# Kernel tuning notes

Measured on AMD Instinct MI355X. Metric: run time of the kernel, lower is better.

The kernel has to match this reference:

```python
import jax, jax.numpy as jnp
import numpy as np

NUM_HEADS = 8
DIM = 256
SCALE = (DIM // NUM_HEADS) ** -0.5  # head_dim = dim // nhead = 32


def setup_inputs() -> dict:
    key = jax.random.key(0)
    k1, k2, k3, k4, k5 = jax.random.split(key, 5)
    B, N = 1, 4096
    qk = jax.random.normal(k1, (B, N, 3 * DIM), dtype=jnp.float32)
    v_cls = jax.random.normal(k2, (B, N, 2 * DIM), dtype=jnp.float32)
    masks = jax.random.uniform(k3, (B, N, N), dtype=jnp.float32)
    # torch Linear weights stored as [in, out] for x @ W
    W_qk = jax.random.normal(k4, (3 * DIM, 6 * DIM), dtype=jnp.float32) * (3 * DIM) ** -0.5
    W_v = jax.random.normal(k5, (2 * DIM, 2 * DIM), dtype=jnp.float32) * (2 * DIM) ** -0.5
    return {"qk": qk, "v_cls": v_cls, "masks": masks, "W_qk": W_qk, "W_v": W_v}


def reference(qk, v_cls, masks, W_qk, W_v):
    B, N, C_qk = qk.shape
    C_cls = v_cls.shape[-1]
    H = NUM_HEADS
    hd_qk = C_qk // H   # 96
    hd_v = C_cls // H   # 64

    # qk projection: [B,N,6*dim] -> (2,B,H,N,hd_qk)
    proj = (qk @ W_qk).reshape(B, N, 2, H, hd_qk).transpose(2, 0, 3, 1, 4)
    q, k = proj[0], proj[1]                      # [B,H,N,hd_qk]
    v = (v_cls @ W_v).reshape(B, N, H, hd_v).transpose(0, 2, 1, 3)  # [B,H,N,hd_v]

    attn = jnp.einsum('bhnd,bhmd->bhnm', q, k) * SCALE
    attn = jax.nn.softmax(attn, axis=-1)

    # post-softmax mask-mul and renorm by mask-sum and head count
    m = masks[:, None]                           # [B,1,N,N] broadcast over heads
    attn = attn * m / (H * jnp.sum(m, axis=-1, keepdims=True))
    # attn_drop with p=0.0 is identity in eval

    x_cls = jnp.einsum('bhnm,bhmd->bhnd', attn, v)
    return x_cls.transpose(0, 2, 1, 3).reshape(B, N, C_cls)
```

## Files before the change

kernel.cpp:

```cpp
#include <hip/hip_runtime.h>

typedef __attribute__((ext_vector_type(8))) _Float16 half8;
typedef __attribute__((ext_vector_type(4))) _Float16 half4;
typedef __attribute__((ext_vector_type(2))) _Float16 half2;
typedef __attribute__((ext_vector_type(2))) __fp16 fp16x2;
typedef __attribute__((ext_vector_type(4))) float f32x4;

#define N_SEQ 4096
#define HD_QK 96
#define HD_V  64
#define NHEADS 8
#define QSCALE 0.25505545556f
#define ESHIFT 8.0f

union PKC { fp16x2 p; half2 h; };

__device__ inline half2 pk_cvt(float a, float b) {
    PKC u;
    u.p = __builtin_amdgcn_cvt_pkrtz(a, b);
    return u.h;
}

__device__ inline half8 cvt8(float4 a, float4 b) {
    half8 h;
    h[0] = (_Float16)a.x; h[1] = (_Float16)a.y; h[2] = (_Float16)a.z; h[3] = (_Float16)a.w;
    h[4] = (_Float16)b.x; h[5] = (_Float16)b.y; h[6] = (_Float16)b.z; h[7] = (_Float16)b.w;
    return h;
}

__device__ inline void cast_blk(const float* __restrict__ in, _Float16* __restrict__ out,
                                int blk, int t) {
    size_t i = ((size_t)blk * 256 + t) * 8;
    float4 a = *(const float4*)(in + i);
    float4 b = *(const float4*)(in + i + 4);
    *(half8*)(out + i) = cvt8(a, b);
}

__global__ __launch_bounds__(256) void prep(
    const float* __restrict__ qk, const float* __restrict__ v_cls,
    const float* __restrict__ masks, const float* __restrict__ W_qk,
    const float* __restrict__ W_v,
    _Float16* __restrict__ Xh, _Float16* __restrict__ Vch,
    _Float16* __restrict__ Msw, float* __restrict__ Msum,
    _Float16* __restrict__ Wqkt, _Float16* __restrict__ Wvt)
{
    __shared__ float tile[32][33];
    const int bx = blockIdx.x, t = threadIdx.x;
    if (bx < 1536) {
        cast_blk(qk, Xh, bx, t);
    } else if (bx < 2560) {
        cast_blk(v_cls, Vch, bx - 1536, t);
    } else if (bx < 3968) {
        const bool big = bx < 3712;
        const int id = big ? bx - 2560 : bx - 3712;
        const int nx = big ? 48 : 16;
        const int C = big ? 1536 : 512, R = big ? 768 : 512;
        const float* in = big ? W_qk : W_v;
        _Float16* out = big ? Wqkt : Wvt;
        int cx = id % nx, cy = id / nx;
        int tx = t & 31, ty = t >> 5;
        int c0 = cx * 32, r0 = cy * 32;
        for (int k = 0; k < 4; k++)
            tile[ty + 8 * k][tx] = in[(size_t)(r0 + ty + 8 * k) * C + c0 + tx];
        __syncthreads();
        for (int k = 0; k < 4; k++)
            out[(size_t)(c0 + ty + 8 * k) * R + r0 + tx] = (_Float16)tile[tx][ty + 8 * k];
    } else {
        const int m = bx - 3968;
        const int q = m >> 1;
        const int k0 = (m & 1) * 2048 + t * 8;
        const float* src = masks + (size_t)q * N_SEQ + k0;
        float4 a = *(const float4*)src;
        float4 b = *(const float4*)(src + 4);
        const int q0b = q >> 6, l15 = q & 15, nt = (q >> 4) & 3;
        const int kb = k0 >> 6, wsl = (k0 >> 4) & 3, qd = (k0 >> 2) & 3;
        _Float16* dst = Msw + ((size_t)(q0b * 64 + kb) * 4 + wsl) * 1024
                            + l15 * 64 + qd * 16 + nt * 4;
        half4 h0 = {(_Float16)a.x, (_Float16)a.y, (_Float16)a.z, (_Float16)a.w};
        half4 h1 = {(_Float16)b.x, (_Float16)b.y, (_Float16)b.z, (_Float16)b.w};
        *(half4*)dst = h0;
        *(half4*)(dst + 16) = h1;
        float s = (a.x + a.y) + (a.z + a.w) + (b.x + b.y) + (b.z + b.w);
        for (int off = 1; off < 64; off <<= 1) s += __shfl_xor(s, off);
        if ((t & 63) == 0) atomicAdd(&Msum[q], s);
    }
}

__global__ __launch_bounds__(256) void proj_fused(
    const _Float16* __restrict__ Xh, const _Float16* __restrict__ Vch,
    const _Float16* __restrict__ Wqkt, const _Float16* __restrict__ Wvt,
    _Float16* __restrict__ Qh, _Float16* __restrict__ Kh,
    _Float16* __restrict__ Vtg)
{
    __shared__ _Float16 smem[2 * 128 * 72];
    _Float16 (*Xs)[72] = (_Float16 (*)[72])smem;
    _Float16 (*Ws)[72] = (_Float16 (*)[72])(smem + 128 * 72);

    const int t = threadIdx.x;
    const int lane = t & 63, wv = t >> 6;
    const int quad = lane >> 4, l15 = lane & 15;
    const bool qkmode = blockIdx.x < 12;
    const int n0 = qkmode ? blockIdx.x * 128 : (blockIdx.x - 12) * 128;
    const int row0 = blockIdx.y * 128;
    const int K = qkmode ? 768 : 512;
    const _Float16* X = qkmode ? Xh : Vch;
    const _Float16* Wt = qkmode ? Wqkt : Wvt;

    const int mB = (wv & 1) * 64, nB = (wv >> 1) * 64;
    const int sr = t >> 1, sk = (t & 1) * 32;

    const f32x4 fzero = {0.f, 0.f, 0.f, 0.f};
    f32x4 acc[4][4];
    for (int i = 0; i < 4; i++)
        for (int j = 0; j < 4; j++) acc[i][j] = fzero;

    for (int k0 = 0; k0 < K; k0 += 64) {
        __syncthreads();
        {
            const _Float16* xp = X + (size_t)(row0 + sr) * K + k0 + sk;
            *(half8*)&Xs[sr][sk]      = *(const half8*)xp;
            *(half8*)&Xs[sr][sk + 8]  = *(const half8*)(xp + 8);
            *(half8*)&Xs[sr][sk + 16] = *(const half8*)(xp + 16);
            *(half8*)&Xs[sr][sk + 24] = *(const half8*)(xp + 24);
            const _Float16* wp = Wt + (size_t)(n0 + sr) * K + k0 + sk;
            *(half8*)&Ws[sr][sk]      = *(const half8*)wp;
            *(half8*)&Ws[sr][sk + 8]  = *(const half8*)(wp + 8);
            *(half8*)&Ws[sr][sk + 16] = *(const half8*)(wp + 16);
            *(half8*)&Ws[sr][sk + 24] = *(const half8*)(wp + 24);
        }
        __syncthreads();
        for (int c = 0; c < 2; c++) {
            half8 af[4], bf[4];
            for (int i = 0; i < 4; i++)
                af[i] = *(const half8*)&Xs[mB + 16 * i + l15][c * 32 + quad * 8];
            for (int j = 0; j < 4; j++)
                bf[j] = *(const half8*)&Ws[nB + 16 * j + l15][c * 32 + quad * 8];
            for (int i = 0; i < 4; i++)
                for (int j = 0; j < 4; j++)
                    acc[i][j] = __builtin_amdgcn_mfma_f32_16x16x32_f16(af[i], bf[j], acc[i][j], 0, 0, 0);
        }
    }

    __syncthreads();
    _Float16 (*Ct)[136] = (_Float16 (*)[136])smem;
    for (int j = 0; j < 4; j++) {
        int col = n0 + nB + 16 * j + l15;
        float scl = (qkmode && col < 768) ? QSCALE : 1.0f;
        for (int i = 0; i < 4; i++)
            for (int r = 0; r < 4; r++)
                Ct[mB + 16 * i + quad * 4 + r][nB + 16 * j + l15] =
                    (_Float16)(acc[i][j][r] * scl);
    }
    __syncthreads();

    if (qkmode) {
        for (int e = 0; e < 8; e++) {
            int id = e * 256 + t;
            int row = id >> 4, cc = id & 15;
            int col = n0 + cc * 8;
            int w = col >= 768 ? 1 : 0;
            int rem = col - w * 768;
            int h = rem / 96, d = rem - h * 96;
            _Float16* dst = w ? Kh : Qh;
            *(half8*)&dst[((size_t)h * N_SEQ + row0 + row) * HD_QK + d] =
                *(const half8*)&Ct[row][cc * 8];
        }
    } else {
        for (int e = 0; e < 4; e++) {
            int id = e * 256 + t;
            int col = id >> 3, rc = id & 7;
            int c = n0 + col;
            int h = c >> 6, d = c & 63;
            half8 v0, v1;
            for (int k = 0; k < 8; k++) {
                v0[k] = Ct[rc * 16 + k][col];
                v1[k] = Ct[rc * 16 + 8 + k][col];
            }
            _Float16* dst = &Vtg[((size_t)h * HD_V + d) * N_SEQ + row0 + rc * 16];
            *(half8*)dst = v0;
            *(half8*)(dst + 8) = v1;
        }
    }
}

__global__ __launch_bounds__(256, 3) void flash_attn(
    const _Float16* __restrict__ Qh, const _Float16* __restrict__ Kh,
    const _Float16* __restrict__ Vtg, const _Float16* __restrict__ Msw,
    _Float16* __restrict__ Owsh, float* __restrict__ Lws)
{
    __shared__ __align__(16) float Ob[2][64][68];
    __shared__ float Lb[2][64];

    const int t = threadIdx.x;
    const int lane = t & 63, w = t >> 6;
    const int quad = lane >> 4, l15 = lane & 15;
    const int bx = blockIdx.x;
    const int q0b = bx & 63;
    const int hz = bx >> 6;
    const int head = hz & 7;
    const int z = hz >> 3;
    const int q0 = q0b * 64;
    const int kb0 = 21 * z, kbE = (z == 2) ? 64 : kb0 + 21;

    half8 qf[3][4];
    for (int nt = 0; nt < 4; nt++) {
        const _Float16* qp = Qh + ((size_t)head * N_SEQ + q0 + 16 * nt + l15) * HD_QK + 8 * quad;
        for (int c = 0; c < 3; c++)
            qf[c][nt] = *(const half8*)(qp + 32 * c);
    }

    const _Float16* kbase = Kh + ((size_t)head * N_SEQ + 16 * w + l15) * HD_QK + 8 * quad;
    const _Float16* vbase = Vtg + ((size_t)head * HD_V + l15) * N_SEQ + 16 * w + 4 * quad;
    const _Float16* mbase = Msw + ((size_t)(q0b * 64 + kb0) * 4 + w) * 1024
                                + (l15 * 4 + quad) * 16;

    const f32x4 fzero = {0.f, 0.f, 0.f, 0.f};
    f32x4 oacc[4][4];
    for (int nt = 0; nt < 4; nt++)
        for (int v = 0; v < 4; v++) oacc[nt][v] = fzero;
    float lsum[4] = {0.f, 0.f, 0.f, 0.f};

    half8 kf[3];
    half4 vf[4];
    half8 m01, m23;
    {
        const _Float16* kp = kbase + (size_t)kb0 * 64 * HD_QK;
        for (int c = 0; c < 3; c++) kf[c] = *(const half8*)(kp + 32 * c);
        const _Float16* vp = vbase + kb0 * 64;
        for (int v = 0; v < 4; v++) vf[v] = *(const half4*)(vp + (size_t)(16 * v) * N_SEQ);
        m01 = *(const half8*)mbase;
        m23 = *(const half8*)(mbase + 8);
    }

    for (int kb = kb0; kb < kbE; kb++) {
        const int kn = (kb + 1 < kbE) ? kb + 1 : kb;

        f32x4 sT[4];
        for (int nt = 0; nt < 4; nt++) sT[nt] = fzero;
        for (int c = 0; c < 3; c++)
            for (int nt = 0; nt < 4; nt++)
                sT[nt] = __builtin_amdgcn_mfma_f32_16x16x32_f16(kf[c], qf[c][nt], sT[nt], 0, 0, 0);
        {
            const _Float16* kp = kbase + (size_t)kn * 64 * HD_QK;
            for (int c = 0; c < 3; c++) kf[c] = *(const half8*)(kp + 32 * c);
        }

        half4 af[4];
        {
            half2 mh[8];
            for (int i = 0; i < 4; i++) {
                mh[i]     = half2{m01[2 * i], m01[2 * i + 1]};
                mh[4 + i] = half2{m23[2 * i], m23[2 * i + 1]};
            }
            for (int nt = 0; nt < 4; nt++) {
                float p0 = exp2f(sT[nt][0] - ESHIFT);
                float p1 = exp2f(sT[nt][1] - ESHIFT);
                float p2 = exp2f(sT[nt][2] - ESHIFT);
                float p3 = exp2f(sT[nt][3] - ESHIFT);
                lsum[nt] += (p0 + p1) + (p2 + p3);
                half2 lo = pk_cvt(p0, p1) * mh[2 * nt];
                half2 hi = pk_cvt(p2, p3) * mh[2 * nt + 1];
                af[nt] = half4{lo[0], lo[1], hi[0], hi[1]};
            }
        }
        {
            const _Float16* mp = mbase + (size_t)(kn - kb0) * 4096;
            m01 = *(const half8*)mp;
            m23 = *(const half8*)(mp + 8);
        }

        for (int nt = 0; nt < 4; nt++)
            for (int v = 0; v < 4; v++)
                oacc[nt][v] = __builtin_amdgcn_mfma_f32_16x16x16f16(af[nt], vf[v], oacc[nt][v], 0, 0, 0);
        {
            const _Float16* vp = vbase + kn * 64;
            for (int v = 0; v < 4; v++) vf[v] = *(const half4*)(vp + (size_t)(16 * v) * N_SEQ);
        }
    }

    for (int nt = 0; nt < 4; nt++) {
        lsum[nt] += __shfl_xor(lsum[nt], 16);
        lsum[nt] += __shfl_xor(lsum[nt], 32);
    }

    if (w & 1) {
        for (int nt = 0; nt < 4; nt++) {
            for (int v = 0; v < 4; v++)
                for (int r = 0; r < 4; r++)
                    Ob[w >> 1][16 * nt + 4 * quad + r][16 * v + l15] = oacc[nt][v][r];
            if (quad == 0) Lb[w >> 1][16 * nt + l15] = lsum[nt];
        }
    }
    __syncthreads();
    if (!(w & 1)) {
        for (int nt = 0; nt < 4; nt++) {
            for (int v = 0; v < 4; v++)
                for (int r = 0; r < 4; r++)
                    Ob[w >> 1][16 * nt + 4 * quad + r][16 * v + l15] += oacc[nt][v][r];
            if (quad == 0) Lb[w >> 1][16 * nt + l15] += lsum[nt];
        }
    }
    __syncthreads();

    {
        int row = t >> 2, c0 = (t & 3) * 16;
        _Float16* obase = Owsh + (size_t)z * N_SEQ * 512 + (size_t)(q0 + row) * 512
                          + head * HD_V + c0;
        for (int g = 0; g < 2; g++) {
            half8 h;
            for (int j = 0; j < 8; j++)
                h[j] = (_Float16)(Ob[0][row][c0 + 8 * g + j] + Ob[1][row][c0 + 8 * g + j]);
            *(half8*)(obase + 8 * g) = h;
        }
        if (t < 64)
            Lws[((size_t)z * NHEADS + head) * N_SEQ + q0 + t] = Lb[0][t] + Lb[1][t];
    }
}

__global__ __launch_bounds__(256) void finalize(
    const _Float16* __restrict__ Owsh, const float* __restrict__ Lws,
    const float* __restrict__ Msum, float* __restrict__ out)
{
    const size_t ZSTR = (size_t)N_SEQ * 512;
    size_t o = ((size_t)blockIdx.x * 256 + threadIdx.x) * 8;
    int q = (int)(o >> 9);
    int head = (int)((o & 511) >> 6);
    half8 p0 = *(const half8*)(Owsh + o);
    half8 p1 = *(const half8*)(Owsh + ZSTR + o);
    half8 p2 = *(const half8*)(Owsh + 2 * ZSTR + o);
    float l = Lws[(size_t)head * N_SEQ + q]
            + Lws[((size_t)NHEADS + head) * N_SEQ + q]
            + Lws[((size_t)2 * NHEADS + head) * N_SEQ + q];
    float inv = 1.0f / (l * (float)NHEADS * Msum[q]);
    float4 r0, r1;
    r0.x = ((float)p0[0] + (float)p1[0] + (float)p2[0]) * inv;
    r0.y = ((float)p0[1] + (float)p1[1] + (float)p2[1]) * inv;
    r0.z = ((float)p0[2] + (float)p1[2] + (float)p2[2]) * inv;
    r0.w = ((float)p0[3] + (float)p1[3] + (float)p2[3]) * inv;
    r1.x = ((float)p0[4] + (float)p1[4] + (float)p2[4]) * inv;
    r1.y = ((float)p0[5] + (float)p1[5] + (float)p2[5]) * inv;
    r1.z = ((float)p0[6] + (float)p1[6] + (float)p2[6]) * inv;
    r1.w = ((float)p0[7] + (float)p1[7] + (float)p2[7]) * inv;
    *(float4*)(out + o) = r0;
    *(float4*)(out + o + 4) = r1;
}

extern "C" void kernel_launch(void* const* d_in, const int* in_sizes, int n_in,
                              void* d_out, int out_size, void* d_ws, size_t ws_size,
                              hipStream_t stream) {
    const float* qk    = (const float*)d_in[0];
    const float* v_cls = (const float*)d_in[1];
    const float* masks = (const float*)d_in[2];
    const float* W_qk  = (const float*)d_in[3];
    const float* W_v   = (const float*)d_in[4];
    float* out = (float*)d_out;

    char* wsp = (char*)d_ws;
    _Float16* Xh   = (_Float16*)(wsp);
    _Float16* Vch  = (_Float16*)(wsp + (size_t)6291456);
    _Float16* Wqkt = (_Float16*)(wsp + (size_t)10485760);
    _Float16* Wvt  = (_Float16*)(wsp + (size_t)12845056);
    _Float16* Owsh = (_Float16*)(wsp);
    size_t off = 13631488;
    auto allocB = [&](size_t bytes) { char* p = wsp + off; off += (bytes + 255) & ~(size_t)255; return p; };
    _Float16* Qh   = (_Float16*)allocB((size_t)NHEADS * N_SEQ * HD_QK * 2);
    _Float16* Kh   = (_Float16*)allocB((size_t)NHEADS * N_SEQ * HD_QK * 2);
    _Float16* Vtg  = (_Float16*)allocB((size_t)NHEADS * HD_V * N_SEQ * 2);
    _Float16* Msw  = (_Float16*)allocB((size_t)N_SEQ * N_SEQ * 2);
    float*    Msum = (float*)allocB((size_t)N_SEQ * 4);
    float*    Lws  = (float*)allocB((size_t)3 * NHEADS * N_SEQ * 4);
    (void)ws_size;

    dim3 blk(256);
    (void)hipMemsetAsync(Msum, 0, N_SEQ * sizeof(float), stream);
    prep<<<dim3(12160), blk, 0, stream>>>(
        qk, v_cls, masks, W_qk, W_v, Xh, Vch, Msw, Msum, Wqkt, Wvt);

    proj_fused<<<dim3(16, N_SEQ / 128), blk, 0, stream>>>(
        Xh, Vch, Wqkt, Wvt, Qh, Kh, Vtg);

    flash_attn<<<dim3(1536), blk, 0, stream>>>(
        Qh, Kh, Vtg, Msw, Owsh, Lws);

    finalize<<<dim3((N_SEQ * 512) / (256 * 8)), blk, 0, stream>>>(
        Owsh, Lws, Msum, out);
}
```

Measured before the change: 280.1 us.

## Rework mask prep tiling, shrink projection tiles with prefetch, split attention four ways

The mask conversion now processes whole 64x64 tiles through shared memory, so global writes are coalesced and one atomic is issued per row quarter instead of per wavefront. The projection kernel uses 64-row tiles with register prefetch of the next K slice and a higher occupancy hint. Flash attention splits the key range into four equal chunks instead of three uneven ones and raises occupancy to 4 blocks per CU. Finalize reduces over four partials. The workspace offset grows to hold the larger partial buffer. Risks are more partial traffic in finalize and register pressure under the tighter launch bounds.

```diff
diff --git a/kernel.cpp b/kernel.cpp
--- a/kernel.cpp
+++ b/kernel.cpp
@@ -12,8 +12,10 @@
 #define NHEADS 8
 #define QSCALE 0.25505545556f
 #define ESHIFT 8.0f
+#define NZ 4
 
 union PKC { fp16x2 p; half2 h; };
+union H8H2 { half8 v; half2 h2[4]; };
 
 __device__ inline half2 pk_cvt(float a, float b) {
     PKC u;
@@ -45,6 +47,7 @@
     _Float16* __restrict__ Wqkt, _Float16* __restrict__ Wvt)
 {
     __shared__ float tile[32][33];
+    __shared__ _Float16 Ml[64][68];
     const int bx = blockIdx.x, t = threadIdx.x;
     if (bx < 1536) {
         cast_blk(qk, Xh, bx, t);
@@ -66,76 +69,104 @@
         for (int k = 0; k < 4; k++)
             out[(size_t)(c0 + ty + 8 * k) * R + r0 + tx] = (_Float16)tile[tx][ty + 8 * k];
     } else {
-        const int m = bx - 3968;
-        const int q = m >> 1;
-        const int k0 = (m & 1) * 2048 + t * 8;
-        const float* src = masks + (size_t)q * N_SEQ + k0;
-        float4 a = *(const float4*)src;
-        float4 b = *(const float4*)(src + 4);
-        const int q0b = q >> 6, l15 = q & 15, nt = (q >> 4) & 3;
-        const int kb = k0 >> 6, wsl = (k0 >> 4) & 3, qd = (k0 >> 2) & 3;
-        _Float16* dst = Msw + ((size_t)(q0b * 64 + kb) * 4 + wsl) * 1024
-                            + l15 * 64 + qd * 16 + nt * 4;
-        half4 h0 = {(_Float16)a.x, (_Float16)a.y, (_Float16)a.z, (_Float16)a.w};
-        half4 h1 = {(_Float16)b.x, (_Float16)b.y, (_Float16)b.z, (_Float16)b.w};
-        *(half4*)dst = h0;
-        *(half4*)(dst + 16) = h1;
-        float s = (a.x + a.y) + (a.z + a.w) + (b.x + b.y) + (b.z + b.w);
-        for (int off = 1; off < 64; off <<= 1) s += __shfl_xor(s, off);
-        if ((t & 63) == 0) atomicAdd(&Msum[q], s);
-    }
-}
-
-__global__ __launch_bounds__(256) void proj_fused(
+        const int b = bx - 3968;
+        const int q0b6 = b >> 6, kb = b & 63;
+        const int qr = t >> 2, ks = t & 3;
+        const float* src = masks + (size_t)(q0b6 * 64 + qr) * N_SEQ + kb * 64 + ks * 16;
+        float4 a0 = *(const float4*)src;
+        float4 a1 = *(const float4*)(src + 4);
+        float4 a2 = *(const float4*)(src + 8);
+        float4 a3 = *(const float4*)(src + 12);
+        *(half8*)&Ml[qr][ks * 16]     = cvt8(a0, a1);
+        *(half8*)&Ml[qr][ks * 16 + 8] = cvt8(a2, a3);
+        float s = ((a0.x + a0.y) + (a0.z + a0.w)) + ((a1.x + a1.y) + (a1.z + a1.w))
+                + ((a2.x + a2.y) + (a2.z + a2.w)) + ((a3.x + a3.y) + (a3.z + a3.w));
+        s += __shfl_xor(s, 1);
+        s += __shfl_xor(s, 2);
+        if ((t & 3) == 0) atomicAdd(&Msum[q0b6 * 64 + qr], s);
+        __syncthreads();
+        const int wsl = t >> 6, l15 = (t >> 2) & 15, quad = t & 3;
+        _Float16* dst = Msw + ((size_t)(q0b6 * 64 + kb) * 4 + wsl) * 1024
+                            + l15 * 64 + quad * 16;
+        half8 o0, o1;
+        for (int nt = 0; nt < 2; nt++)
+            for (int j = 0; j < 4; j++)
+                o0[nt * 4 + j] = Ml[nt * 16 + l15][wsl * 16 + quad * 4 + j];
+        for (int nt = 2; nt < 4; nt++)
+            for (int j = 0; j < 4; j++)
+                o1[(nt - 2) * 4 + j] = Ml[nt * 16 + l15][wsl * 16 + quad * 4 + j];
+        *(half8*)dst = o0;
+        *(half8*)(dst + 8) = o1;
+    }
+}
+
+__global__ __launch_bounds__(256, 4) void proj_fused(
     const _Float16* __restrict__ Xh, const _Float16* __restrict__ Vch,
     const _Float16* __restrict__ Wqkt, const _Float16* __restrict__ Wvt,
     _Float16* __restrict__ Qh, _Float16* __restrict__ Kh,
     _Float16* __restrict__ Vtg)
 {
-    __shared__ _Float16 smem[2 * 128 * 72];
+    __shared__ _Float16 smem[64 * 72 + 128 * 72];
     _Float16 (*Xs)[72] = (_Float16 (*)[72])smem;
-    _Float16 (*Ws)[72] = (_Float16 (*)[72])(smem + 128 * 72);
+    _Float16 (*Ws)[72] = (_Float16 (*)[72])(smem + 64 * 72);
 
     const int t = threadIdx.x;
     const int lane = t & 63, wv = t >> 6;
     const int quad = lane >> 4, l15 = lane & 15;
     const bool qkmode = blockIdx.x < 12;
     const int n0 = qkmode ? blockIdx.x * 128 : (blockIdx.x - 12) * 128;
-    const int row0 = blockIdx.y * 128;
+    const int row0 = blockIdx.y * 64;
     const int K = qkmode ? 768 : 512;
     const _Float16* X = qkmode ? Xh : Vch;
     const _Float16* Wt = qkmode ? Wqkt : Wvt;
 
-    const int mB = (wv & 1) * 64, nB = (wv >> 1) * 64;
-    const int sr = t >> 1, sk = (t & 1) * 32;
+    const int mB = (wv & 1) * 32, nB = (wv >> 1) * 64;
+    const int xr = t >> 2, xc = (t & 3) * 16;
+    const int wr = t >> 1, wc = (t & 1) * 32;
 
     const f32x4 fzero = {0.f, 0.f, 0.f, 0.f};
-    f32x4 acc[4][4];
-    for (int i = 0; i < 4; i++)
+    f32x4 acc[2][4];
+    for (int i = 0; i < 2; i++)
         for (int j = 0; j < 4; j++) acc[i][j] = fzero;
+
+    half8 xg0, xg1, wg0, wg1, wg2, wg3;
+    {
+        const _Float16* xp = X + (size_t)(row0 + xr) * K + xc;
+        xg0 = *(const half8*)xp;
+        xg1 = *(const half8*)(xp + 8);
+        const _Float16* wp = Wt + (size_t)(n0 + wr) * K + wc;
+        wg0 = *(const half8*)wp;
+        wg1 = *(const half8*)(wp + 8);
+        wg2 = *(const half8*)(wp + 16);
+        wg3 = *(const half8*)(wp + 24);
+    }
 
     for (int k0 = 0; k0 < K; k0 += 64) {
         __syncthreads();
-        {
-            const _Float16* xp = X + (size_t)(row0 + sr) * K + k0 + sk;
-            *(half8*)&Xs[sr][sk]      = *(const half8*)xp;
-            *(half8*)&Xs[sr][sk + 8]  = *(const half8*)(xp + 8);
-            *(half8*)&Xs[sr][sk + 16] = *(const half8*)(xp + 16);
-            *(half8*)&Xs[sr][sk + 24] = *(const half8*)(xp + 24);
-            const _Float16* wp = Wt + (size_t)(n0 + sr) * K + k0 + sk;
-            *(half8*)&Ws[sr][sk]      = *(const half8*)wp;
-            *(half8*)&Ws[sr][sk + 8]  = *(const half8*)(wp + 8);
-            *(half8*)&Ws[sr][sk + 16] = *(const half8*)(wp + 16);
-            *(half8*)&Ws[sr][sk + 24] = *(const half8*)(wp + 24);
-        }
+        *(half8*)&Xs[xr][xc]     = xg0;
+        *(half8*)&Xs[xr][xc + 8] = xg1;
+        *(half8*)&Ws[wr][wc]      = wg0;
+        *(half8*)&Ws[wr][wc + 8]  = wg1;
+        *(half8*)&Ws[wr][wc + 16] = wg2;
+        *(half8*)&Ws[wr][wc + 24] = wg3;
         __syncthreads();
+        if (k0 + 64 < K) {
+            const _Float16* xp = X + (size_t)(row0 + xr) * K + k0 + 64 + xc;
+            xg0 = *(const half8*)xp;
+            xg1 = *(const half8*)(xp + 8);
+            const _Float16* wp = Wt + (size_t)(n0 + wr) * K + k0 + 64 + wc;
+            wg0 = *(const half8*)wp;
+            wg1 = *(const half8*)(wp + 8);
+            wg2 = *(const half8*)(wp + 16);
+            wg3 = *(const half8*)(wp + 24);
+        }
         for (int c = 0; c < 2; c++) {
-            half8 af[4], bf[4];
-            for (int i = 0; i < 4; i++)
+            half8 af[2], bf[4];
+            for (int i = 0; i < 2; i++)
                 af[i] = *(const half8*)&Xs[mB + 16 * i + l15][c * 32 + quad * 8];
             for (int j = 0; j < 4; j++)
                 bf[j] = *(const half8*)&Ws[nB + 16 * j + l15][c * 32 + quad * 8];
-            for (int i = 0; i < 4; i++)
+            for (int i = 0; i < 2; i++)
                 for (int j = 0; j < 4; j++)
                     acc[i][j] = __builtin_amdgcn_mfma_f32_16x16x32_f16(af[i], bf[j], acc[i][j], 0, 0, 0);
         }
@@ -146,7 +177,7 @@
     for (int j = 0; j < 4; j++) {
         int col = n0 + nB + 16 * j + l15;
         float scl = (qkmode && col < 768) ? QSCALE : 1.0f;
-        for (int i = 0; i < 4; i++)
+        for (int i = 0; i < 2; i++)
             for (int r = 0; r < 4; r++)
                 Ct[mB + 16 * i + quad * 4 + r][nB + 16 * j + l15] =
                     (_Float16)(acc[i][j][r] * scl);
@@ -154,7 +185,7 @@
     __syncthreads();
 
     if (qkmode) {
-        for (int e = 0; e < 8; e++) {
+        for (int e = 0; e < 4; e++) {
             int id = e * 256 + t;
             int row = id >> 4, cc = id & 15;
             int col = n0 + cc * 8;
@@ -166,9 +197,9 @@
                 *(const half8*)&Ct[row][cc * 8];
         }
     } else {
-        for (int e = 0; e < 4; e++) {
+        for (int e = 0; e < 2; e++) {
             int id = e * 256 + t;
-            int col = id >> 3, rc = id & 7;
+            int col = id >> 2, rc = id & 3;
             int c = n0 + col;
             int h = c >> 6, d = c & 63;
             half8 v0, v1;
@@ -183,7 +214,7 @@
     }
 }
 
-__global__ __launch_bounds__(256, 3) void flash_attn(
+__global__ __launch_bounds__(256, 4) void flash_attn(
     const _Float16* __restrict__ Qh, const _Float16* __restrict__ Kh,
     const _Float16* __restrict__ Vtg, const _Float16* __restrict__ Msw,
     _Float16* __restrict__ Owsh, float* __restrict__ Lws)
@@ -200,7 +231,7 @@
     const int head = hz & 7;
     const int z = hz >> 3;
     const int q0 = q0b * 64;
-    const int kb0 = 21 * z, kbE = (z == 2) ? 64 : kb0 + 21;
+    const int kb0 = 16 * z, kbE = kb0 + 16;
 
     half8 qf[3][4];
     for (int nt = 0; nt < 4; nt++) {
@@ -222,14 +253,14 @@
 
     half8 kf[3];
     half4 vf[4];
-    half8 m01, m23;
+    H8H2 mu0, mu1;
     {
         const _Float16* kp = kbase + (size_t)kb0 * 64 * HD_QK;
         for (int c = 0; c < 3; c++) kf[c] = *(const half8*)(kp + 32 * c);
         const _Float16* vp = vbase + kb0 * 64;
         for (int v = 0; v < 4; v++) vf[v] = *(const half4*)(vp + (size_t)(16 * v) * N_SEQ);
-        m01 = *(const half8*)mbase;
-        m23 = *(const half8*)(mbase + 8);
+        mu0.v = *(const half8*)mbase;
+        mu1.v = *(const half8*)(mbase + 8);
     }
 
     for (int kb = kb0; kb < kbE; kb++) {
@@ -246,27 +277,22 @@
         }
 
         half4 af[4];
-        {
-            half2 mh[8];
-            for (int i = 0; i < 4; i++) {
-                mh[i]     = half2{m01[2 * i], m01[2 * i + 1]};
-                mh[4 + i] = half2{m23[2 * i], m23[2 * i + 1]};
-            }
-            for (int nt = 0; nt < 4; nt++) {
-                float p0 = exp2f(sT[nt][0] - ESHIFT);
-                float p1 = exp2f(sT[nt][1] - ESHIFT);
-                float p2 = exp2f(sT[nt][2] - ESHIFT);
-                float p3 = exp2f(sT[nt][3] - ESHIFT);
-                lsum[nt] += (p0 + p1) + (p2 + p3);
-                half2 lo = pk_cvt(p0, p1) * mh[2 * nt];
-                half2 hi = pk_cvt(p2, p3) * mh[2 * nt + 1];
-                af[nt] = half4{lo[0], lo[1], hi[0], hi[1]};
-            }
+        for (int nt = 0; nt < 4; nt++) {
+            const half2* mh = (nt < 2) ? mu0.h2 : mu1.h2;
+            const int mb = (nt & 1) * 2;
+            float p0 = exp2f(sT[nt][0] - ESHIFT);
+            float p1 = exp2f(sT[nt][1] - ESHIFT);
+            float p2 = exp2f(sT[nt][2] - ESHIFT);
+            float p3 = exp2f(sT[nt][3] - ESHIFT);
+            lsum[nt] += (p0 + p1) + (p2 + p3);
+            half2 lo = pk_cvt(p0, p1) * mh[mb];
+            half2 hi = pk_cvt(p2, p3) * mh[mb + 1];
+            af[nt] = half4{lo[0], lo[1], hi[0], hi[1]};
         }
         {
             const _Float16* mp = mbase + (size_t)(kn - kb0) * 4096;
-            m01 = *(const half8*)mp;
-            m23 = *(const half8*)(mp + 8);
+            mu0.v = *(const half8*)mp;
+            mu1.v = *(const half8*)(mp + 8);
         }
 
         for (int nt = 0; nt < 4; nt++)
@@ -325,22 +351,18 @@
     size_t o = ((size_t)blockIdx.x * 256 + threadIdx.x) * 8;
     int q = (int)(o >> 9);
     int head = (int)((o & 511) >> 6);
-    half8 p0 = *(const half8*)(Owsh + o);
-    half8 p1 = *(const half8*)(Owsh + ZSTR + o);
-    half8 p2 = *(const half8*)(Owsh + 2 * ZSTR + o);
-    float l = Lws[(size_t)head * N_SEQ + q]
-            + Lws[((size_t)NHEADS + head) * N_SEQ + q]
-            + Lws[((size_t)2 * NHEADS + head) * N_SEQ + q];
+    float l = 0.f;
+    for (int z = 0; z < NZ; z++)
+        l += Lws[((size_t)z * NHEADS + head) * N_SEQ + q];
     float inv = 1.0f / (l * (float)NHEADS * Msum[q]);
-    float4 r0, r1;
-    r0.x = ((float)p0[0] + (float)p1[0] + (float)p2[0]) * inv;
-    r0.y = ((float)p0[1] + (float)p1[1] + (float)p2[1]) * inv;
-    r0.z = ((float)p0[2] + (float)p1[2] + (float)p2[2]) * inv;
-    r0.w = ((float)p0[3] + (float)p1[3] + (float)p2[3]) * inv;
-    r1.x = ((float)p0[4] + (float)p1[4] + (float)p2[4]) * inv;
-    r1.y = ((float)p0[5] + (float)p1[5] + (float)p2[5]) * inv;
-    r1.z = ((float)p0[6] + (float)p1[6] + (float)p2[6]) * inv;
-    r1.w = ((float)p0[7] + (float)p1[7] + (float)p2[7]) * inv;
+    float acc[8];
+    for (int j = 0; j < 8; j++) acc[j] = 0.f;
+    for (int z = 0; z < NZ; z++) {
+        half8 p = *(const half8*)(Owsh + (size_t)z * ZSTR + o);
+        for (int j = 0; j < 8; j++) acc[j] += (float)p[j];
+    }
+    float4 r0 = {acc[0] * inv, acc[1] * inv, acc[2] * inv, acc[3] * inv};
+    float4 r1 = {acc[4] * inv, acc[5] * inv, acc[6] * inv, acc[7] * inv};
     *(float4*)(out + o) = r0;
     *(float4*)(out + o + 4) = r1;
 }
@@ -361,25 +383,25 @@
     _Float16* Wqkt = (_Float16*)(wsp + (size_t)10485760);
     _Float16* Wvt  = (_Float16*)(wsp + (size_t)12845056);
     _Float16* Owsh = (_Float16*)(wsp);
-    size_t off = 13631488;
+    size_t off = 16777216;
     auto allocB = [&](size_t bytes) { char* p = wsp + off; off += (bytes + 255) & ~(size_t)255; return p; };
     _Float16* Qh   = (_Float16*)allocB((size_t)NHEADS * N_SEQ * HD_QK * 2);
     _Float16* Kh   = (_Float16*)allocB((size_t)NHEADS * N_SEQ * HD_QK * 2);
     _Float16* Vtg  = (_Float16*)allocB((size_t)NHEADS * HD_V * N_SEQ * 2);
     _Float16* Msw  = (_Float16*)allocB((size_t)N_SEQ * N_SEQ * 2);
     float*    Msum = (float*)allocB((size_t)N_SEQ * 4);
-    float*    Lws  = (float*)allocB((size_t)3 * NHEADS * N_SEQ * 4);
+    float*    Lws  = (float*)allocB((size_t)NZ * NHEADS * N_SEQ * 4);
     (void)ws_size;
 
     dim3 blk(256);
     (void)hipMemsetAsync(Msum, 0, N_SEQ * sizeof(float), stream);
-    prep<<<dim3(12160), blk, 0, stream>>>(
+    prep<<<dim3(8064), blk, 0, stream>>>(
         qk, v_cls, masks, W_qk, W_v, Xh, Vch, Msw, Msum, Wqkt, Wvt);
 
-    proj_fused<<<dim3(16, N_SEQ / 128), blk, 0, stream>>>(
+    proj_fused<<<dim3(16, N_SEQ / 64), blk, 0, stream>>>(
         Xh, Vch, Wqkt, Wvt, Qh, Kh, Vtg);
 
-    flash_attn<<<dim3(1536), blk, 0, stream>>>(
+    flash_attn<<<dim3(64 * NHEADS * NZ), blk, 0, stream>>>(
         Qh, Kh, Vtg, Msw, Owsh, Lws);
 
     finalize<<<dim3((N_SEQ * 512) / (256 * 8)), blk, 0, stream>>>(
```

Measured after the change: 425.5 us. 1.52x slower.
